# Kernel optimization log

Hardware: AMD Instinct MI355X
Metric: run time of the kernel (lower is better)

Reference implementation:

```python
import jax, jax.numpy as jnp
import numpy as np

B, S, D = 2, 2048, 2048
H, KV, HD = 32, 8, 64
REP = H // KV  # query heads per kv head
SCALE = np.float32(1.0 / np.sqrt(HD))


def setup_inputs() -> dict:
    key = jax.random.key(0)
    ks = jax.random.split(key, 5)
    x = jax.random.normal(ks[0], (B, S, D), dtype=jnp.float32)
    # RoPE tables: standard rotate_half convention, cos/sin shape [S, HD]
    inv_freq = 1.0 / (10000.0 ** (jnp.arange(0, HD, 2, dtype=jnp.float32) / HD))
    freqs = jnp.outer(jnp.arange(S, dtype=jnp.float32), inv_freq)  # [S, HD/2]
    emb = jnp.concatenate([freqs, freqs], axis=-1)  # [S, HD]
    cos, sin = jnp.cos(emb), jnp.sin(emb)
    std = np.float32(0.02)
    Wq = jax.random.normal(ks[1], (D, H * HD), dtype=jnp.float32) * std
    Wk = jax.random.normal(ks[2], (D, KV * HD), dtype=jnp.float32) * std
    Wv = jax.random.normal(ks[3], (D, KV * HD), dtype=jnp.float32) * std
    Wo = jax.random.normal(ks[4], (H * HD, D), dtype=jnp.float32) * std
    return {"x": x, "cos": cos, "sin": sin, "Wq": Wq, "Wk": Wk, "Wv": Wv, "Wo": Wo}


def _rotate_half(u):
    u1, u2 = jnp.split(u, 2, axis=-1)
    return jnp.concatenate([-u2, u1], axis=-1)


def reference(x, cos, sin, Wq, Wk, Wv, Wo):
    # projections -> [B, heads, S, HD]
    q = (x @ Wq).reshape(B, S, H, HD).transpose(0, 2, 1, 3)
    k = (x @ Wk).reshape(B, S, KV, HD).transpose(0, 2, 1, 3)
    v = (x @ Wv).reshape(B, S, KV, HD).transpose(0, 2, 1, 3)
    # RoPE on q and k (cos/sin broadcast over batch & head dims)
    c, s = cos[None, None], sin[None, None]
    q = q * c + _rotate_half(q) * s
    k = k * c + _rotate_half(k) * s
    # GQA: group query heads per kv head instead of materializing repeat_kv
    qg = q.reshape(B, KV, REP, S, HD)
    scores = jnp.einsum('bgrqd,bgkd->bgrqk', qg, k) * SCALE  # [B,KV,REP,S,S]
    causal = jnp.tril(jnp.ones((S, S), dtype=bool))
    scores = jnp.where(causal, scores, jnp.float32(-1e30))
    attn = jax.nn.softmax(scores, axis=-1)
    out = jnp.einsum('bgrqk,bgkd->bgrqd', attn, v)  # [B,KV,REP,S,HD]
    out = out.reshape(B, H, S, HD).transpose(0, 2, 1, 3).reshape(B, S, H * HD)
    return out @ Wo
```

## Files before the change

kernel.cpp:

```cpp
#include <hip/hip_runtime.h>

typedef unsigned short u16;
typedef __bf16 bfx8 __attribute__((ext_vector_type(8)));
typedef float f32x4 __attribute__((ext_vector_type(4)));
typedef float f32x16 __attribute__((ext_vector_type(16)));

#define MFMA16(a,b,c) __builtin_amdgcn_mfma_f32_16x16x32_bf16(a,b,c,0,0,0)
#define MFMA32(a,b,c) __builtin_amdgcn_mfma_f32_32x32x16_bf16(a,b,c,0,0,0)

__device__ __forceinline__ u16 f2bf(float f) {
  union { float f; unsigned u; } v; v.f = f;
  unsigned r = v.u + 0x7fffu + ((v.u >> 16) & 1u);
  return (u16)(r >> 16);
}

__device__ __forceinline__ unsigned cvtpk(float lo, float hi) {
  unsigned r;
  asm("v_cvt_pk_bf16_f32 %0, %1, %2" : "=v"(r) : "v"(lo), "v"(hi));
  return r;
}

__device__ __forceinline__ void swap32(unsigned &a, unsigned &b) {
  asm("v_permlane32_swap_b32 %0, %1" : "+v"(a), "+v"(b));
}

__device__ __forceinline__ void gld16(const void* g, void* l) {
  __builtin_amdgcn_global_load_lds(
      (const __attribute__((address_space(1))) unsigned int*)g,
      (__attribute__((address_space(3))) unsigned int*)l, 16, 0, 0);
}


__global__ void afrag_k(const float* __restrict__ in, u16* __restrict__ Af) {
  int i = blockIdx.x * 256 + threadIdx.x;
  int sm = i >> 8, d0 = (i & 255) * 8;
  const float* p = in + (size_t)sm * 2048 + d0;
  float4 a = *(const float4*)p;
  float4 b = *(const float4*)(p + 4);
  union { u16 h[8]; uint4 u; } o;
  o.h[0]=f2bf(a.x); o.h[1]=f2bf(a.y); o.h[2]=f2bf(a.z); o.h[3]=f2bf(a.w);
  o.h[4]=f2bf(b.x); o.h[5]=f2bf(b.y); o.h[6]=f2bf(b.z); o.h[7]=f2bf(b.w);
  int mt = sm >> 4, kt = d0 >> 5, lp = (sm & 15) + ((d0 >> 3) & 3) * 16;
  *(uint4*)(Af + ((size_t)(mt * 64 + kt) * 512 + lp * 8)) = o.u;
}

__global__ void bfrag_k(const float* __restrict__ W, u16* __restrict__ Bf,
                        int N, int ntoff) {
  __shared__ float tile[32][72];
  int nb = blockIdx.x, kb = blockIdx.y;
  int t = threadIdx.x;
  int r = t >> 3, c8 = (t & 7) * 8;
  const float* src = W + (size_t)(kb * 32 + r) * N + nb * 64 + c8;
  *(float4*)&tile[r][c8]     = *(const float4*)src;
  *(float4*)&tile[r][c8 + 4] = *(const float4*)(src + 4);
  __syncthreads();
  int fb = t >> 6, l = t & 63;
  int nn = fb * 16 + (l & 15), k0 = (l >> 4) * 8;
  union { u16 h[8]; uint4 u; } o;
  #pragma unroll
  for (int j = 0; j < 8; j++) o.h[j] = f2bf(tile[k0 + j][nn]);
  *(uint4*)(Bf + ((size_t)((ntoff + nb * 4 + fb) * 64 + kb) * 512 + l * 8)) = o.u;
}

__global__ __launch_bounds__(256, 3) void gemm_qkv(
    const u16* __restrict__ Af, const u16* __restrict__ Bf,
    const float* __restrict__ cosT, const float* __restrict__ sinT,
    u16* __restrict__ Qf, u16* __restrict__ Kf, u16* __restrict__ Vf) {
  __shared__ u16 lds[2 * 20 * 512];
  const int tid = threadIdx.x, lane = tid & 63, w = tid >> 6;
  const int lrow = lane & 15, lg = lane >> 4;
  const int nwg = gridDim.x;
  const int per = nwg >> 3;
  const int swz = ((int)blockIdx.x & 7) * per + ((int)blockIdx.x >> 3);
  const int bm = swz / 12, bn = swz % 12;
  const int bm4 = bm * 4, bn16 = bn * 16;
  const int KT = 64;

  f32x4 acc[4][4] = {};
  u16* buf0 = lds;
  u16* buf1 = lds + 20 * 512;

  auto stageB = [&](int s, u16* dst) {
    #pragma unroll
    for (int j = 0; j < 4; j++) {
      int ng = w * 4 + j;
      gld16(Bf + ((size_t)(bn16 + ng) * KT + s) * 512 + lane * 8,
            dst + (4 + ng) * 512);
    }
  };
  auto stageA = [&](int s, u16* dst) {
    gld16(Af + ((size_t)(bm4 + w) * KT + s) * 512 + lane * 8,
          dst + w * 512);
  };

  stageB(0, buf0); stageA(0, buf0);
  stageB(1, buf1); stageA(1, buf1);
  asm volatile("s_waitcnt vmcnt(5)" ::: "memory");
  __builtin_amdgcn_s_barrier();

  bfx8 ar[2], br[4];
  for (int t = 0; t < KT; t++) {
    u16* rb = (t & 1) ? buf1 : buf0;
    const int s2 = (t + 2 < KT) ? t + 2 : 0;
    #pragma unroll
    for (int i = 0; i < 2; i++)
      ar[i] = *(const bfx8*)(rb + i * 512 + lane * 8);
    #pragma unroll
    for (int j = 0; j < 4; j++)
      br[j] = *(const bfx8*)(rb + (4 + w * 4 + j) * 512 + lane * 8);
    asm volatile("s_waitcnt lgkmcnt(0)" ::: "memory");
    __builtin_amdgcn_s_barrier();
    stageB(s2, rb);
    __builtin_amdgcn_s_setprio(1);
    #pragma unroll
    for (int i = 0; i < 2; i++)
      #pragma unroll
      for (int j = 0; j < 4; j++)
        acc[i][j] = MFMA16(ar[i], br[j], acc[i][j]);
    __builtin_amdgcn_s_setprio(0);
    __builtin_amdgcn_s_barrier();
    #pragma unroll
    for (int i = 0; i < 2; i++)
      ar[i] = *(const bfx8*)(rb + (2 + i) * 512 + lane * 8);
    asm volatile("s_waitcnt lgkmcnt(0)" ::: "memory");
    __builtin_amdgcn_s_barrier();
    stageA(s2, rb);
    __builtin_amdgcn_s_setprio(1);
    #pragma unroll
    for (int i = 0; i < 2; i++)
      #pragma unroll
      for (int j = 0; j < 4; j++)
        acc[2 + i][j] = MFMA16(ar[i], br[j], acc[2 + i][j]);
    __builtin_amdgcn_s_setprio(0);
    asm volatile("s_waitcnt vmcnt(5)" ::: "memory");
    __builtin_amdgcn_s_barrier();
  }
  asm volatile("s_waitcnt vmcnt(0)" ::: "memory");
  __builtin_amdgcn_s_barrier();

  const int hh = bn * 4 + w;
  const int m0 = bm * 64;
  u16* otw = lds + w * 2048;
  char* otb = (char*)otw;

  #pragma unroll
  for (int half = 0; half < 2; half++) {
    const int rowbase = m0 + half * 32;
    const int bb = rowbase >> 11;
    const int s0 = rowbase & 2047;
    if (hh < 40) {
      const float qsc = (hh < 32) ? 0.18033688f : 1.0f;
      #pragma unroll
      for (int mgl = 0; mgl < 2; mgl++) {
        const int mg = half * 2 + mgl;
        #pragma unroll
        for (int ng = 0; ng < 2; ng++) {
          const int d1 = ng * 16 + lrow;
          #pragma unroll
          for (int r = 0; r < 4; r++) {
            int s = s0 + mgl * 16 + lg * 4 + r;
            float a  = acc[mg][ng][r];
            float a2 = acc[mg][ng + 2][r];
            float c1 = cosT[s * 64 + d1],      s1v = sinT[s * 64 + d1];
            float c2 = cosT[s * 64 + d1 + 32], s2v = sinT[s * 64 + d1 + 32];
            float o1 = (a * c1 - a2 * s1v) * qsc;
            float o2 = (a2 * c2 + a * s2v) * qsc;
            int srow = mgl * 16 + lg * 4 + r;
            int swzb = (srow & 7) << 4;
            *(u16*)(otb + ((srow * 128 + d1 * 2) ^ swzb)) = f2bf(o1);
            *(u16*)(otb + ((srow * 128 + (d1 + 32) * 2) ^ swzb)) = f2bf(o2);
          }
        }
      }
      const int qt = s0 >> 5;
      u16* dst = (hh < 32)
          ? Qf + ((size_t)(bb * 32 + hh) * 64 + qt) * 2048
          : Kf + ((size_t)(bb * 8 + (hh - 32)) * 64 + qt) * 2048;
      const int srw = lane & 31;
      const int d0 = (lane >> 5) * 8;
      #pragma unroll
      for (int ks = 0; ks < 4; ks++) {
        int byte = ((srw * 128 + (ks * 16 + d0) * 2)) ^ ((srw & 7) << 4);
        uint4 v = *(uint4*)(otb + byte);
        *(uint4*)(dst + ks * 512 + lane * 8) = v;
      }
    } else {
      #pragma unroll
      for (int mgl = 0; mgl < 2; mgl++) {
        const int mg = half * 2 + mgl;
        #pragma unroll
        for (int ng = 0; ng < 4; ng++) {
          const int d = ng * 16 + lrow;
          #pragma unroll
          for (int r = 0; r < 4; r++) {
            int srow = mgl * 16 + lg * 4 + r;
            *(u16*)(otb + ((srow * 128 + d * 2) ^ ((srow & 7) << 4))) =
                f2bf(acc[mg][ng][r]);
          }
        }
      }
      const int kt = s0 >> 6;
      const int g = hh - 40;
      u16* dst = Vf + ((size_t)(bb * 8 + g) * 32 + kt) * 4096;
      const int d = lane & 31;
      const int hi8 = (lane >> 5) * 8;
      #pragma unroll
      for (int ks2 = 0; ks2 < 2; ks2++) {
        const int ks = half * 2 + ks2;
        #pragma unroll
        for (int sub = 0; sub < 2; sub++) {
          const int dd = sub * 32 + d;
          union { u16 h[8]; uint4 u; } o;
          #pragma unroll
          for (int j = 0; j < 8; j++) {
            int srow = ks2 * 16 + hi8 + j;
            o.h[j] = *(u16*)(otb + ((srow * 128 + dd * 2) ^ ((srow & 7) << 4)));
          }
          *(uint4*)(dst + (sub * 4 + ks) * 512 + lane * 8) = o.u;
        }
      }
    }
    __builtin_amdgcn_s_barrier();
  }
}

__global__ __launch_bounds__(256, 3) void gemm8p(
    const u16* __restrict__ Af, const u16* __restrict__ Bf,
    float* __restrict__ C, int N, int KT, int nbx) {
  __shared__ u16 lds[2 * 20 * 512];
  const int tid = threadIdx.x, lane = tid & 63, w = tid >> 6;
  const int lrow = lane & 15, lg = lane >> 4;
  const int nwg = gridDim.x;
  const int per = nwg >> 3;
  const int swz = ((int)blockIdx.x & 7) * per + ((int)blockIdx.x >> 3);
  const int bm = swz / nbx, bn = swz % nbx;
  const int bm4 = bm * 4, bn16 = bn * 16;
  const int T = KT;

  f32x4 acc[4][4] = {};
  u16* buf0 = lds;
  u16* buf1 = lds + 20 * 512;

  auto stageB = [&](int s, u16* dst) {
    #pragma unroll
    for (int j = 0; j < 4; j++) {
      int ng = w * 4 + j;
      gld16(Bf + ((size_t)(bn16 + ng) * KT + s) * 512 + lane * 8,
            dst + (4 + ng) * 512);
    }
  };
  auto stageA = [&](int s, u16* dst) {
    gld16(Af + ((size_t)(bm4 + w) * KT + s) * 512 + lane * 8,
          dst + w * 512);
  };

  stageB(0, buf0); stageA(0, buf0);
  stageB(1, buf1); stageA(1, buf1);
  asm volatile("s_waitcnt vmcnt(5)" ::: "memory");
  __builtin_amdgcn_s_barrier();

  bfx8 ar[2], br[4];
  for (int t = 0; t < T; t++) {
    u16* rb = (t & 1) ? buf1 : buf0;
    const int s2 = (t + 2 < T) ? t + 2 : 0;
    #pragma unroll
    for (int i = 0; i < 2; i++)
      ar[i] = *(const bfx8*)(rb + i * 512 + lane * 8);
    #pragma unroll
    for (int j = 0; j < 4; j++)
      br[j] = *(const bfx8*)(rb + (4 + w * 4 + j) * 512 + lane * 8);
    asm volatile("s_waitcnt lgkmcnt(0)" ::: "memory");
    __builtin_amdgcn_s_barrier();
    stageB(s2, rb);
    __builtin_amdgcn_s_setprio(1);
    #pragma unroll
    for (int i = 0; i < 2; i++)
      #pragma unroll
      for (int j = 0; j < 4; j++)
        acc[i][j] = MFMA16(ar[i], br[j], acc[i][j]);
    __builtin_amdgcn_s_setprio(0);
    __builtin_amdgcn_s_barrier();
    #pragma unroll
    for (int i = 0; i < 2; i++)
      ar[i] = *(const bfx8*)(rb + (2 + i) * 512 + lane * 8);
    asm volatile("s_waitcnt lgkmcnt(0)" ::: "memory");
    __builtin_amdgcn_s_barrier();
    stageA(s2, rb);
    __builtin_amdgcn_s_setprio(1);
    #pragma unroll
    for (int i = 0; i < 2; i++)
      #pragma unroll
      for (int j = 0; j < 4; j++)
        acc[2 + i][j] = MFMA16(ar[i], br[j], acc[2 + i][j]);
    __builtin_amdgcn_s_setprio(0);
    asm volatile("s_waitcnt vmcnt(5)" ::: "memory");
    __builtin_amdgcn_s_barrier();
  }
  asm volatile("s_waitcnt vmcnt(0)" ::: "memory");

  const int m0 = bm * 64, n0 = bn * 256 + w * 64;
  #pragma unroll
  for (int mg = 0; mg < 4; mg++) {
    int row = m0 + mg * 16 + lg * 4;
    #pragma unroll
    for (int ng = 0; ng < 4; ng++) {
      int col = n0 + ng * 16 + lrow;
      float* cp = C + (size_t)row * N + col;
      #pragma unroll
      for (int r = 0; r < 4; r++) cp[(size_t)r * N] = acc[mg][ng][r];
    }
  }
}

__global__ __launch_bounds__(256, 2) void attn_k(
    const u16* __restrict__ Qf, const u16* __restrict__ Kf,
    const u16* __restrict__ Vf, u16* __restrict__ Aof)
{
  __shared__ u16 ot[4][32 * 64];
  const int tid = threadIdx.x, lane = tid & 63, w = tid >> 6;
  const int h = blockIdx.y, b = blockIdx.z;
  const int kvh = h >> 2;
  const int ql = lane & 31, hi = lane >> 5;
  const int qrA = blockIdx.x * 4 + w;

  const u16* Qh = Qf + (size_t)(b * 32 + h) * 131072;
  const u16* Kp = Kf + (size_t)(b * 8 + kvh) * 131072 + lane * 8;
  const u16* Vp = Vf + (size_t)(b * 8 + kvh) * 131072 + lane * 8;

  #pragma unroll
  for (int half = 0; half < 2; half++) {
    const int qr = half ? qrA : 63 - qrA;
    const int q0 = qr * 32;
    const int qg = q0 + ql;
    const int nkt = qr / 2 + 1;

    bfx8 qf[4];
    #pragma unroll
    for (int ks = 0; ks < 4; ks++)
      qf[ks] = *(const bfx8*)(Qh + (size_t)qr * 2048 + ks * 512 + lane * 8);

    f32x16 oacc0 = {}, oacc1 = {};
    float m2 = -3.0e38f;
    float lsum = 0.f;

    const u16* Kt = Kp;
    const u16* Vt = Vp;
    bfx8 ka[8];
    #pragma unroll
    for (int i = 0; i < 8; i++)
      ka[i] = *(const bfx8*)(Kt + i * 512);

    #pragma unroll 2
    for (int kt = 0; kt < nkt; kt++) {
      const int kb = kt * 64;
      bfx8 va[8];
      #pragma unroll
      for (int i = 0; i < 8; i++)
        va[i] = *(const bfx8*)(Vt + i * 512);
      f32x16 st0 = {}, st1 = {};
      #pragma unroll
      for (int ks = 0; ks < 4; ks++) {
        st0 = MFMA32(ka[ks], qf[ks], st0);
        st1 = MFMA32(ka[4 + ks], qf[ks], st1);
      }
      const u16* Kn = (kt + 1 < nkt) ? Kt + 4096 : Kp;
      bfx8 kn[8];
      #pragma unroll
      for (int i = 0; i < 8; i++)
        kn[i] = *(const bfx8*)(Kn + i * 512);
      if (kt == nkt - 1) {
        #pragma unroll
        for (int r = 0; r < 16; r++) {
          int crow = (r & 3) + 8 * (r >> 2) + 4 * hi;
          if (kb + crow > qg) st0[r] = -3.0e38f;
          if (kb + 32 + crow > qg) st1[r] = -3.0e38f;
        }
      }
      float mx[16];
      #pragma unroll
      for (int r = 0; r < 16; r++) mx[r] = fmaxf(st0[r], st1[r]);
      #pragma unroll
      for (int s = 8; s > 0; s >>= 1)
        #pragma unroll
        for (int r = 0; r < s; r++) mx[r] = fmaxf(mx[r], mx[r + s]);
      float tm = fmaxf(mx[0], __shfl_xor(mx[0], 32));
      float mnew = fmaxf(m2, tm);
      if (!__all(tm <= m2 + 8.0f)) {
        float corr = exp2f(m2 - mnew);
        lsum *= corr;
        #pragma unroll
        for (int i = 0; i < 16; i++) { oacc0[i] *= corr; oacc1[i] *= corr; }
        m2 = mnew;
      }
      #pragma unroll
      for (int r = 0; r < 16; r++) { st0[r] = exp2f(st0[r] - m2); }
      #pragma unroll
      for (int r = 0; r < 16; r++) { st1[r] = exp2f(st1[r] - m2); }
      float sm[16];
      #pragma unroll
      for (int r = 0; r < 16; r++) sm[r] = st0[r] + st1[r];
      #pragma unroll
      for (int s = 8; s > 0; s >>= 1)
        #pragma unroll
        for (int r = 0; r < s; r++) sm[r] += sm[r + s];
      lsum += sm[0];
      bfx8 pb[4];
      #pragma unroll
      for (int ks = 0; ks < 4; ks++) {
        int o = (ks & 1) * 8;
        unsigned X = cvtpk(ks < 2 ? st0[o + 0] : st1[o + 0], ks < 2 ? st0[o + 1] : st1[o + 1]);
        unsigned Z = cvtpk(ks < 2 ? st0[o + 2] : st1[o + 2], ks < 2 ? st0[o + 3] : st1[o + 3]);
        unsigned Y = cvtpk(ks < 2 ? st0[o + 4] : st1[o + 4], ks < 2 ? st0[o + 5] : st1[o + 5]);
        unsigned W = cvtpk(ks < 2 ? st0[o + 6] : st1[o + 6], ks < 2 ? st0[o + 7] : st1[o + 7]);
        swap32(X, Y);
        swap32(Z, W);
        union { unsigned u[4]; bfx8 v; } uu;
        uu.u[0] = X; uu.u[1] = Z; uu.u[2] = Y; uu.u[3] = W;
        pb[ks] = uu.v;
      }
      #pragma unroll
      for (int ks = 0; ks < 4; ks++) {
        oacc0 = MFMA32(va[ks], pb[ks], oacc0);
        oacc1 = MFMA32(va[4 + ks], pb[ks], oacc1);
      }
      #pragma unroll
      for (int i = 0; i < 8; i++) ka[i] = kn[i];
      Kt += 4096;
      Vt += 4096;
    }
    lsum += __shfl_xor(lsum, 32);
    float inv = 1.f / lsum;
    u16* my = ot[w];
    #pragma unroll
    for (int dt = 0; dt < 2; dt++) {
      #pragma unroll
      for (int g = 0; g < 4; g++) {
        float a0 = (dt ? oacc1[g*4+0] : oacc0[g*4+0]) * inv;
        float a1 = (dt ? oacc1[g*4+1] : oacc0[g*4+1]) * inv;
        float a2 = (dt ? oacc1[g*4+2] : oacc0[g*4+2]) * inv;
        float a3 = (dt ? oacc1[g*4+3] : oacc0[g*4+3]) * inv;
        unsigned w0 = cvtpk(a0, a1), w1 = cvtpk(a2, a3);
        int d = dt * 32 + g * 8 + 4 * hi;
        int byte = (ql * 128 + d * 2) ^ ((ql & 7) << 4);
        *(uint2*)((char*)my + byte) = make_uint2(w0, w1);
      }
    }
    #pragma unroll
    for (int rr = 0; rr < 4; rr++) {
      int q = rr * 8 + (lane >> 3);
      int dk = (lane & 7) * 8;
      int byte = (q * 128 + dk * 2) ^ ((q & 7) << 4);
      uint4 val = *(uint4*)((char*)my + byte);
      int mt = b * 128 + qr * 2 + (q >> 4);
      int ktg = h * 2 + (dk >> 5);
      int lp = (q & 15) + ((dk >> 3) & 3) * 16;
      *(uint4*)(Aof + ((size_t)(mt * 64 + ktg) * 512 + lp * 8)) = val;
    }
  }
}

extern "C" void kernel_launch(void* const* d_in, const int* in_sizes, int n_in,
                              void* d_out, int out_size, void* d_ws, size_t ws_size,
                              hipStream_t stream) {
  const float* x    = (const float*)d_in[0];
  const float* cosT = (const float*)d_in[1];
  const float* sinT = (const float*)d_in[2];
  const float* Wq   = (const float*)d_in[3];
  const float* Wk   = (const float*)d_in[4];
  const float* Wv   = (const float*)d_in[5];
  const float* Wo   = (const float*)d_in[6];
  float* out = (float*)d_out;
  char* ws = (char*)d_ws;

  u16* Af   = (u16*)(ws);
  u16* Bqkv = (u16*)(ws + 16777216);
  u16* Bwo  = (u16*)(ws + 29360128);
  u16* Qf   = (u16*)(ws + 37748736);
  u16* Kf   = (u16*)(ws + 54525952);
  u16* Vf   = (u16*)(ws + 58720256);
  u16* Aof  = (u16*)(ws + 62914560);

  afrag_k<<<4096, 256, 0, stream>>>(x, Af);
  bfrag_k<<<dim3(32, 64), 256, 0, stream>>>(Wq, Bqkv, 2048, 0);
  bfrag_k<<<dim3(8, 64), 256, 0, stream>>>(Wk, Bqkv, 512, 128);
  bfrag_k<<<dim3(8, 64), 256, 0, stream>>>(Wv, Bqkv, 512, 160);
  bfrag_k<<<dim3(32, 64), 256, 0, stream>>>(Wo, Bwo, 2048, 0);

  gemm_qkv<<<768, 256, 0, stream>>>(Af, Bqkv, cosT, sinT, Qf, Kf, Vf);

  attn_k<<<dim3(8, 32, 2), 256, 0, stream>>>(Qf, Kf, Vf, Aof);

  gemm8p<<<512, 256, 0, stream>>>(Aof, Bwo, out, 2048, 64, 8);
}
```

Baseline: 196.6 us.

## Share K/V tiles across waves via double-buffered LDS staging in attention

Each wave previously loaded its own copy of every K/V tile from global memory into registers. The block now loads each 64-key K/V tile once with async global-to-LDS copies into a double buffer, and all four waves read it from shared memory. To make this work, query rows are regrouped so all waves in a block share the same key-tile count, and the causal mask check runs per tile based on position. This cuts redundant global/L2 traffic but adds a block barrier every iteration, extra masked work for waves with shorter rows, and more LDS use that could reduce occupancy.

```diff
diff --git a/kernel.cpp b/kernel.cpp
--- a/kernel.cpp
+++ b/kernel.cpp
@@ -316,23 +316,34 @@
     const u16* __restrict__ Qf, const u16* __restrict__ Kf,
     const u16* __restrict__ Vf, u16* __restrict__ Aof)
 {
+  __shared__ u16 kv[2][16 * 512];
   __shared__ u16 ot[4][32 * 64];
   const int tid = threadIdx.x, lane = tid & 63, w = tid >> 6;
   const int h = blockIdx.y, b = blockIdx.z;
   const int kvh = h >> 2;
   const int ql = lane & 31, hi = lane >> 5;
-  const int qrA = blockIdx.x * 4 + w;
 
   const u16* Qh = Qf + (size_t)(b * 32 + h) * 131072;
-  const u16* Kp = Kf + (size_t)(b * 8 + kvh) * 131072 + lane * 8;
-  const u16* Vp = Vf + (size_t)(b * 8 + kvh) * 131072 + lane * 8;
-
-  #pragma unroll
+  const u16* Kp = Kf + (size_t)(b * 8 + kvh) * 131072;
+  const u16* Vp = Vf + (size_t)(b * 8 + kvh) * 131072;
+
+  auto stage = [&](int kt, int bufi) {
+    u16* dstb = kv[bufi];
+    #pragma unroll
+    for (int j = 0; j < 4; j++) {
+      int blk = w * 4 + j;
+      const u16* src = (blk < 8) ? (Kp + (size_t)kt * 4096 + blk * 512)
+                                 : (Vp + (size_t)kt * 4096 + (blk - 8) * 512);
+      gld16(src + lane * 8, dstb + blk * 512);
+    }
+  };
+
   for (int half = 0; half < 2; half++) {
-    const int qr = half ? qrA : 63 - qrA;
+    const int qb = half ? (int)blockIdx.x : 15 - (int)blockIdx.x;
+    const int qr = qb * 4 + w;
     const int q0 = qr * 32;
     const int qg = q0 + ql;
-    const int nkt = qr / 2 + 1;
+    const int nkt = qb * 2 + 2;
 
     bfx8 qf[4];
     #pragma unroll
@@ -343,32 +354,28 @@
     float m2 = -3.0e38f;
     float lsum = 0.f;
 
-    const u16* Kt = Kp;
-    const u16* Vt = Vp;
-    bfx8 ka[8];
-    #pragma unroll
-    for (int i = 0; i < 8; i++)
-      ka[i] = *(const bfx8*)(Kt + i * 512);
-
-    #pragma unroll 2
+    stage(0, 0);
+    asm volatile("s_waitcnt vmcnt(0)" ::: "memory");
+    __builtin_amdgcn_s_barrier();
+
     for (int kt = 0; kt < nkt; kt++) {
       const int kb = kt * 64;
-      bfx8 va[8];
+      u16* cb = kv[kt & 1];
+      bfx8 ka[8], va[8];
       #pragma unroll
       for (int i = 0; i < 8; i++)
-        va[i] = *(const bfx8*)(Vt + i * 512);
+        ka[i] = *(const bfx8*)(cb + i * 512 + lane * 8);
+      #pragma unroll
+      for (int i = 0; i < 8; i++)
+        va[i] = *(const bfx8*)(cb + (8 + i) * 512 + lane * 8);
+      if (kt + 1 < nkt) stage(kt + 1, (kt + 1) & 1);
       f32x16 st0 = {}, st1 = {};
       #pragma unroll
       for (int ks = 0; ks < 4; ks++) {
         st0 = MFMA32(ka[ks], qf[ks], st0);
         st1 = MFMA32(ka[4 + ks], qf[ks], st1);
       }
-      const u16* Kn = (kt + 1 < nkt) ? Kt + 4096 : Kp;
-      bfx8 kn[8];
-      #pragma unroll
-      for (int i = 0; i < 8; i++)
-        kn[i] = *(const bfx8*)(Kn + i * 512);
-      if (kt == nkt - 1) {
+      if (kb + 63 > qg) {
         #pragma unroll
         for (int r = 0; r < 16; r++) {
           int crow = (r & 3) + 8 * (r >> 2) + 4 * hi;
@@ -423,10 +430,8 @@
         oacc0 = MFMA32(va[ks], pb[ks], oacc0);
         oacc1 = MFMA32(va[4 + ks], pb[ks], oacc1);
       }
-      #pragma unroll
-      for (int i = 0; i < 8; i++) ka[i] = kn[i];
-      Kt += 4096;
-      Vt += 4096;
+      asm volatile("s_waitcnt vmcnt(0)" ::: "memory");
+      __builtin_amdgcn_s_barrier();
     }
     lsum += __shfl_xor(lsum, 32);
     float inv = 1.f / lsum;
```

Result: slower. 200.8 us (+2.1%).
